# Kernel optimization log

Hardware: AMD Instinct MI355X
Metric: run time of the kernel (lower is better)

Reference implementation:

```python
import jax, jax.numpy as jnp
import numpy as np
from jax import lax

B, T = 32, 256
VOCAB, WDIM, MDIM = 50000, 300, 50
HID, NLAYERS, NCLASSES = 512, 2, 3


def _init(key, shape, scale):
    return (jax.random.normal(key, shape, dtype=jnp.float32) * scale)


def setup_inputs() -> dict:
    key = jax.random.key(0)
    ks = jax.random.split(key, 20)
    inputs_seq = jax.random.randint(ks[0], (B, T), 0, VOCAB, dtype=jnp.int32)
    masks = jax.random.randint(ks[1], (B, T), 0, 2, dtype=jnp.int32)
    length = jax.random.randint(ks[2], (B, 1), T // 2, T + 1, dtype=jnp.int32)
    embedding = _init(ks[3], (VOCAB, WDIM), 0.1)
    mask_embedding = _init(ks[4], (2, MDIM), 0.1)
    transition = _init(ks[5], (2, 2), 1.0)
    d_in0 = WDIM + MDIM          # 350
    d_in1 = 2 * HID              # 1024
    w_fw0 = _init(ks[6], (d_in0 + HID, 4 * HID), 0.02)
    b_fw0 = jnp.zeros((4 * HID,), jnp.float32)
    w_bw0 = _init(ks[7], (d_in0 + HID, 4 * HID), 0.02)
    b_bw0 = jnp.zeros((4 * HID,), jnp.float32)
    w_fw1 = _init(ks[8], (d_in1 + HID, 4 * HID), 0.02)
    b_fw1 = jnp.zeros((4 * HID,), jnp.float32)
    w_bw1 = _init(ks[9], (d_in1 + HID, 4 * HID), 0.02)
    b_bw1 = jnp.zeros((4 * HID,), jnp.float32)
    crf_w = _init(ks[10], (2 * HID, 2), 0.02)
    crf_b = jnp.zeros((2,), jnp.float32)
    logits_w = _init(ks[11], (2 * HID, NCLASSES), 0.02)
    logits_b = jnp.zeros((NCLASSES,), jnp.float32)
    return dict(inputs_seq=inputs_seq, masks=masks, length=length,
                embedding=embedding, mask_embedding=mask_embedding,
                transition=transition,
                w_fw0=w_fw0, b_fw0=b_fw0, w_bw0=w_bw0, b_bw0=b_bw0,
                w_fw1=w_fw1, b_fw1=b_fw1, w_bw1=w_bw1, b_bw1=b_bw1,
                crf_w=crf_w, crf_b=crf_b, logits_w=logits_w, logits_b=logits_b)


def _lstm_scan(x, length, W, b):
    """TF LSTMCell (gate order i, j, f, o; forget_bias=1.0) over time.
    Outputs are zeroed and state held past sequence_length (dynamic_rnn semantics)."""
    Bb, Tt, _ = x.shape
    H = W.shape[1] // 4
    zero = jnp.zeros((Bb, H), x.dtype)

    def step(carry, inp):
        h, c = carry
        xt, t = inp
        z = jnp.concatenate([xt, h], axis=-1) @ W + b
        i, j, f, o = jnp.split(z, 4, axis=-1)
        c_new = jax.nn.sigmoid(f + 1.0) * c + jax.nn.sigmoid(i) * jnp.tanh(j)
        h_new = jax.nn.sigmoid(o) * jnp.tanh(c_new)
        m = (t < length)[:, None]
        c = jnp.where(m, c_new, c)
        h = jnp.where(m, h_new, h)
        out = jnp.where(m, h_new, 0.0)
        return (h, c), out

    _, ys = lax.scan(step, (zero, zero), (x.transpose(1, 0, 2), jnp.arange(Tt)))
    return ys.transpose(1, 0, 2)  # [B,T,H]


def _reverse_seq(x, length):
    """tf.reverse_sequence along time: reverse first `length` steps, keep rest."""
    Tt = x.shape[1]
    t = jnp.arange(Tt)[None, :]
    L = length[:, None]
    idx = jnp.where(t < L, L - 1 - t, t)  # [B,T]
    return jnp.take_along_axis(x, idx[:, :, None], axis=1)


def _forward(inputs_seq, masks, length, embedding, mask_embedding, transition,
             lstm_params, crf_w, crf_b, logits_w, logits_b):
    length = length.reshape(-1)  # tf.squeeze
    emb = embedding[inputs_seq]          # [B,T,WDIM]
    memb = mask_embedding[masks]         # [B,T,MDIM]
    out = jnp.concatenate([emb, memb], axis=-1)
    for (wf, bf, wb, bb) in lstm_params:
        fw = _lstm_scan(out, length, wf, bf)
        bw = _reverse_seq(_lstm_scan(_reverse_seq(out, length), length, wb, bb), length)
        out = jnp.concatenate([fw, bw], axis=-1)  # [B,T,2H]

    # CRF forward probabilities over 2 tags
    e = out @ crf_w + crf_b              # [B,T,2] emission scores
    Tt = e.shape[1]
    alpha0 = e[:, 0]

    def crf_step(alpha, inp):
        et, t = inp
        new = jax.nn.logsumexp(alpha[:, :, None] + transition[None], axis=1) + et
        m = (t < length)[:, None]
        alpha = jnp.where(m, new, alpha)
        p = jnp.where(m, jax.nn.softmax(alpha, axis=-1), 0.0)
        return alpha, p

    _, probs_rest = lax.scan(crf_step, alpha0,
                             (e[:, 1:].transpose(1, 0, 2), jnp.arange(1, Tt)))
    p0 = jnp.where((length > 0)[:, None], jax.nn.softmax(alpha0, axis=-1), 0.0)
    probs = jnp.concatenate([p0[None], probs_rest], axis=0).transpose(1, 0, 2)  # [B,T,2]

    crf_out = probs[:, :, -1][:, None, :]            # [B,1,T]
    sentiment_vector = crf_out @ out                  # [B,1,2H]
    logits = jax.nn.softmax(sentiment_vector @ logits_w + logits_b, axis=-1)
    return logits  # [B,1,NCLASSES]


def reference(inputs_seq, masks, length, embedding, mask_embedding, transition,
              w_fw0, b_fw0, w_bw0, b_bw0, w_fw1, b_fw1, w_bw1, b_bw1,
              crf_w, crf_b, logits_w, logits_b):
    lstm_params = [(w_fw0, b_fw0, w_bw0, b_bw0), (w_fw1, b_fw1, w_bw1, b_bw1)]
    return _forward(inputs_seq, masks, length, embedding, mask_embedding,
                    transition, lstm_params, crf_w, crf_b, logits_w, logits_b)
```

## Files before the change

kernel.cpp:

```cpp
#include <hip/hip_runtime.h>
#include <hip/hip_bf16.h>
#include <cstdint>
#include <cstddef>

#define BB 32
#define TT 256
#define HID 512

typedef __attribute__((ext_vector_type(8))) short short8v;
typedef __attribute__((ext_vector_type(4))) float float4v;
typedef __attribute__((ext_vector_type(4))) unsigned int uint4v;

__device__ __forceinline__ float bf2f(unsigned short u) {
  return __uint_as_float(((unsigned int)u) << 16);
}
__device__ __forceinline__ unsigned short f2bf(float f) {
  unsigned int x = __float_as_uint(f);
  x += 0x7fffu + ((x >> 16) & 1u);
  return (unsigned short)(x >> 16);
}

__device__ __forceinline__ void stg4u_cohere(unsigned short* p, uint4v v) {
  asm volatile("global_store_dwordx4 %0, %1, off sc0 sc1"
               :: "v"(p), "v"(v) : "memory");
}
__device__ __forceinline__ void ldg4u_cohere_issue(uint4v& d, const unsigned short* p) {
  asm volatile("global_load_dwordx4 %0, %1, off sc0 sc1"
               : "=v"(d) : "v"(p) : "memory");
}
__device__ __forceinline__ void wait_vm0() {
  asm volatile("s_waitcnt vmcnt(0)" ::: "memory");
  __builtin_amdgcn_sched_barrier(0);
}

__global__ __launch_bounds__(256) void embed_kernel(
    const int* __restrict__ ids, const int* __restrict__ msk,
    const float* __restrict__ emb, const float* __restrict__ memb,
    unsigned short* __restrict__ x0b)
{
  int bt = blockIdx.x;
  int id = ids[bt];
  int m  = msk[bt];
  const float* er = emb  + (size_t)id * 300;
  const float* mr = memb + (size_t)m * 50;
  for (int d = threadIdx.x; d < 384; d += 256) {
    float v = (d < 300) ? er[d] : (d < 350 ? mr[d - 300] : 0.f);
    x0b[(size_t)bt * 384 + d] = f2bf(v);
  }
}

__global__ __launch_bounds__(256) void prep_w(
    const float* __restrict__ W, unsigned short* __restrict__ dst,
    int Kreal, int Kpad)
{
  __shared__ float tile[64][65];
  int tid = threadIdx.x;
  int n0 = blockIdx.x * 64;
  int k0 = blockIdx.y * 64;
#pragma unroll
  for (int i = 0; i < 4; ++i) {
    int e = tid + 256 * i;
    int r = e >> 4, c4 = (e & 15) * 4;
    float4 v = make_float4(0.f, 0.f, 0.f, 0.f);
    if (k0 + r < Kreal) v = *(const float4*)(W + (size_t)(k0 + r) * 2048 + n0 + c4);
    tile[r][c4 + 0] = v.x; tile[r][c4 + 1] = v.y;
    tile[r][c4 + 2] = v.z; tile[r][c4 + 3] = v.w;
  }
  __syncthreads();
  int nl = tid >> 2;
  int kg = (tid & 3) * 16;
  unsigned int pk[4], pk2[4];
#pragma unroll
  for (int jj = 0; jj < 4; ++jj) {
    unsigned short lo = f2bf(tile[kg + jj * 2 + 0][nl]);
    unsigned short hi = f2bf(tile[kg + jj * 2 + 1][nl]);
    pk[jj] = (unsigned int)lo | ((unsigned int)hi << 16);
  }
#pragma unroll
  for (int jj = 0; jj < 4; ++jj) {
    unsigned short lo = f2bf(tile[kg + 8 + jj * 2 + 0][nl]);
    unsigned short hi = f2bf(tile[kg + 8 + jj * 2 + 1][nl]);
    pk2[jj] = (unsigned int)lo | ((unsigned int)hi << 16);
  }
  size_t off = (size_t)(n0 + nl) * Kpad + k0 + kg;
  *(uint4*)(dst + off) = make_uint4(pk[0], pk[1], pk[2], pk[3]);
  *(uint4*)(dst + off + 8) = make_uint4(pk2[0], pk2[1], pk2[2], pk2[3]);
}

__global__ __launch_bounds__(256) void gemm_xproj(
    const unsigned short* __restrict__ A,
    const unsigned short* __restrict__ wxt,
    const float* __restrict__ bias,
    unsigned short* __restrict__ xq,
    int Kpad, int nkb)
{
  __shared__ unsigned short ws_s[128 * 64];
  __shared__ unsigned short xs_s[32 * 64];
  __shared__ float bias_s[128];
  int tid = threadIdx.x;
  int lane = tid & 63;
  int w = tid >> 6;
  int pos = blockIdx.x;
  int n0 = blockIdx.y * 128;
  if (tid < 128) bias_s[tid] = bias[n0 + tid];

  float4v acc[2][2];
#pragma unroll
  for (int i = 0; i < 2; ++i)
#pragma unroll
    for (int j = 0; j < 2; ++j) acc[i][j] = (float4v)0.f;

  int brow = tid >> 3;
  int seg = tid & 7;
  for (int kb = 0; kb < nkb; ++kb) {
    int k0 = kb * 64;
    __syncthreads();
    {
      const unsigned short* src = A + (size_t)(brow * 256 + pos) * Kpad + k0 + seg * 8;
      uint4 v = *(const uint4*)src;
      int o = (brow * 128 + seg * 16) ^ ((brow & 7) << 4);
      *(uint4*)((char*)xs_s + o) = v;
    }
#pragma unroll
    for (int i = 0; i < 4; ++i) {
      int n = i * 32 + brow;
      const unsigned short* src = wxt + (size_t)(n0 + n) * Kpad + k0 + seg * 8;
      uint4 v = *(const uint4*)src;
      int o = (n * 128 + seg * 16) ^ ((n & 7) << 4);
      *(uint4*)((char*)ws_s + o) = v;
    }
    __syncthreads();
#pragma unroll
    for (int kin = 0; kin < 64; kin += 32) {
      int kl = kin + ((lane >> 4) << 3);
      short8v afrag[2], bfrag[2];
#pragma unroll
      for (int nt = 0; nt < 2; ++nt) {
        int nl = w * 32 + nt * 16 + (lane & 15);
        int o = (nl * 128 + kl * 2) ^ ((nl & 7) << 4);
        afrag[nt] = *(const short8v*)((const char*)ws_s + o);
      }
#pragma unroll
      for (int bt = 0; bt < 2; ++bt) {
        int bl = bt * 16 + (lane & 15);
        int o = (bl * 128 + kl * 2) ^ ((bl & 7) << 4);
        bfrag[bt] = *(const short8v*)((const char*)xs_s + o);
      }
#pragma unroll
      for (int nt = 0; nt < 2; ++nt)
#pragma unroll
        for (int bt = 0; bt < 2; ++bt)
          acc[nt][bt] = __builtin_amdgcn_mfma_f32_16x16x32_bf16(
              afrag[nt], bfrag[bt], acc[nt][bt], 0, 0, 0);
    }
  }
  unsigned short* outp = xq + (size_t)pos * 65536;
#pragma unroll
  for (int nt = 0; nt < 2; ++nt) {
#pragma unroll
    for (int bt = 0; bt < 2; ++bt) {
#pragma unroll
      for (int reg = 0; reg < 4; ++reg) {
        int nl = w * 32 + nt * 16 + ((lane >> 4) << 2) + reg;
        int b = bt * 16 + (lane & 15);
        float v = acc[nt][bt][reg] + bias_s[nl];
        outp[(size_t)(n0 + nl) * 32 + b] = f2bf(v);
      }
    }
  }
}

__global__ __launch_bounds__(256) void lstm_mfma(
    const unsigned short* __restrict__ xq_fw, const unsigned short* __restrict__ xq_bw,
    const unsigned short* __restrict__ whT_fw, const unsigned short* __restrict__ whT_bw,
    const int* __restrict__ length,
    unsigned short* __restrict__ out,
    unsigned short* __restrict__ hT,
    float* __restrict__ cbuf,
    int* __restrict__ flags,
    int t0, int t1)
{
  extern __shared__ char smem[];
  float* zs = (float*)(smem + 65536);
  unsigned short* hb_st = (unsigned short*)(smem + 69632);
  unsigned short* ob_st = (unsigned short*)(smem + 70144);
  int tid = threadIdx.x;
  int wg = blockIdx.x;
  int dir = wg >> 6;
  int widx = wg & 63;
  int u0 = widx << 3;
  const unsigned short* xq = dir ? xq_bw : xq_fw;
  const unsigned short* whT = dir ? whT_bw : whT_fw;
  unsigned short* hbase = hT + (size_t)dir * 32768;
  int* dirflags = flags + dir * 2048;
  int* myflag = dirflags + widx * 32;

  {
    int r = tid >> 3;
    int q = r >> 3, d = r & 7;
    const unsigned short* src = whT + (size_t)(q * 512 + u0 + d) * 512 + (tid & 7) * 8;
    int ob = r * 1024 + (tid & 7) * 16;
    int sw = (r & 7) << 4;
#pragma unroll
    for (int i = 0; i < 8; ++i) {
      uint4 v = *(const uint4*)(src + i * 64);
      *(uint4*)(smem + ((ob + i * 128) ^ sw)) = v;
    }
  }

  int lane = tid & 63;
  int w = tid >> 6;
  int wr = w >> 1, wc = w & 1;
  int arow = wr * 16 + (lane & 15);
  int bcol = wc * 16 + (lane & 15);
  int chunk16 = (lane >> 4) << 4;
  int asw = (arow & 7) << 4;
  int bsw = (bcol & 7) << 4;
  int fu = tid >> 5;
  int fb = tid & 31;
  int ug = u0 + fu;
  int L = length[fb];
  float creg = 0.f;

  for (int t = t0; t < t1; ++t) {
    int sl = dir ? (TT - 1 - t) : t;
    const unsigned short* hTr_g = hbase + (size_t)(t & 1) * 16384;
    unsigned short* hTw_g = hbase + (size_t)((t & 1) ^ 1) * 16384;

    const unsigned short* xr = xq + (size_t)sl * 65536 + (size_t)ug * 32 + fb;
    float xv0 = bf2f(xr[0]);
    float xv1 = bf2f(xr[16384]);
    float xv2 = bf2f(xr[32768]);
    float xv3 = bf2f(xr[49152]);

    {
      int row = tid >> 3;
      const unsigned short* src = hTr_g + row * 512 + (tid & 7) * 8;
      uint4v r0, r1, r2, r3, r4, r5, r6, r7;
      ldg4u_cohere_issue(r0, src + 0 * 64);
      ldg4u_cohere_issue(r1, src + 1 * 64);
      ldg4u_cohere_issue(r2, src + 2 * 64);
      ldg4u_cohere_issue(r3, src + 3 * 64);
      ldg4u_cohere_issue(r4, src + 4 * 64);
      ldg4u_cohere_issue(r5, src + 5 * 64);
      ldg4u_cohere_issue(r6, src + 6 * 64);
      ldg4u_cohere_issue(r7, src + 7 * 64);
      wait_vm0();
      int ob = 32768 + row * 1024 + (tid & 7) * 16;
      int sw = (row & 7) << 4;
      *(uint4v*)(smem + ((ob + 0 * 128) ^ sw)) = r0;
      *(uint4v*)(smem + ((ob + 1 * 128) ^ sw)) = r1;
      *(uint4v*)(smem + ((ob + 2 * 128) ^ sw)) = r2;
      *(uint4v*)(smem + ((ob + 3 * 128) ^ sw)) = r3;
      *(uint4v*)(smem + ((ob + 4 * 128) ^ sw)) = r4;
      *(uint4v*)(smem + ((ob + 5 * 128) ^ sw)) = r5;
      *(uint4v*)(smem + ((ob + 6 * 128) ^ sw)) = r6;
      *(uint4v*)(smem + ((ob + 7 * 128) ^ sw)) = r7;
    }
    __syncthreads();

    float4v acc = (float4v)0.f;
#pragma unroll
    for (int ks = 0; ks < 16; ++ks) {
      int kb = ks * 64 + chunk16;
      short8v af = *(const short8v*)(smem + (size_t)arow * 1024 + (kb ^ asw));
      short8v bf = *(const short8v*)(smem + 32768 + (size_t)bcol * 1024 + (kb ^ bsw));
      acc = __builtin_amdgcn_mfma_f32_16x16x32_bf16(af, bf, acc, 0, 0, 0);
    }
#pragma unroll
    for (int r = 0; r < 4; ++r) {
      int row = wr * 16 + ((lane >> 4) << 2) + r;
      zs[row * 32 + bcol] = acc[r];
    }
    __syncthreads();

    {
      bool active = sl < L;
      float z0 = zs[(0 * 8 + fu) * 32 + fb] + xv0;
      float z1 = zs[(1 * 8 + fu) * 32 + fb] + xv1;
      float z2 = zs[(2 * 8 + fu) * 32 + fb] + xv2;
      float z3 = zs[(3 * 8 + fu) * 32 + fb] + xv3;
      int ho = 32768 + fb * 1024 + ((ug * 2) ^ ((fb & 7) << 4));
      float h_old = bf2f(*(const unsigned short*)(smem + ho));
      float c_old = cbuf ? cbuf[dir * 16384 + ug * 32 + fb] : creg;
      float si = 1.f / (1.f + expf(-z0));
      float sj = tanhf(z1);
      float sf = 1.f / (1.f + expf(-(z2 + 1.f)));
      float so = 1.f / (1.f + expf(-z3));
      float cn = sf * c_old + si * sj;
      float hn = so * tanhf(cn);
      if (active) {
        if (cbuf) cbuf[dir * 16384 + ug * 32 + fb] = cn; else creg = cn;
      }
      hb_st[fb * 8 + fu] = f2bf(active ? hn : h_old);
      ob_st[fb * 8 + fu] = f2bf(active ? hn : 0.f);
    }
    __syncthreads();

    if (tid < 32) {
      uint4v hv = *(const uint4v*)(hb_st + tid * 8);
      stg4u_cohere(hTw_g + tid * 512 + u0, hv);
      uint4v ov = *(const uint4v*)(ob_st + tid * 8);
      *(uint4v*)(out + (size_t)(tid * TT + sl) * 1024 + dir * 512 + u0) = ov;
    }

    if (t1 - t0 > 1) {
      wait_vm0();
      __syncthreads();
      if (tid == 0) {
        __hip_atomic_store(myflag, t + 1, __ATOMIC_RELAXED,
                           __HIP_MEMORY_SCOPE_AGENT);
      }
      if (tid < 64) {
        int* f = dirflags + tid * 32;
        while (__hip_atomic_load(f, __ATOMIC_RELAXED,
                                 __HIP_MEMORY_SCOPE_AGENT) < t + 1) {
          __builtin_amdgcn_s_sleep(1);
        }
      }
      __syncthreads();
    }
  }
}

__global__ __launch_bounds__(256) void crf_final(
    const unsigned short* __restrict__ out1,
    const float* __restrict__ crf_w, const float* __restrict__ crf_b,
    const float* __restrict__ trans,
    const int* __restrict__ length,
    const float* __restrict__ lw, const float* __restrict__ lb,
    float* __restrict__ dout)
{
  __shared__ float e[TT][2];
  __shared__ float pw[TT];
  __shared__ float sv[1024];
  __shared__ float red[256];
  int b = blockIdx.x, tid = threadIdx.x;
  int lane = tid & 63, w = tid >> 6;
  const unsigned short* ob = out1 + (size_t)b * TT * 1024;
  for (int t = w; t < TT; t += 4) {
    float a0 = 0.f, a1 = 0.f;
    for (int i = 0; i < 16; ++i) {
      int d = lane + i * 64;
      float v = bf2f(ob[(size_t)t * 1024 + d]);
      a0 += v * crf_w[d * 2];
      a1 += v * crf_w[d * 2 + 1];
    }
    for (int off = 32; off; off >>= 1) {
      a0 += __shfl_down(a0, off);
      a1 += __shfl_down(a1, off);
    }
    if (lane == 0) { e[t][0] = a0 + crf_b[0]; e[t][1] = a1 + crf_b[1]; }
  }
  __syncthreads();
  if (tid == 0) {
    int L = length[b];
    float t00 = trans[0], t01 = trans[1], t10 = trans[2], t11 = trans[3];
    float a0 = e[0][0], a1 = e[0][1];
    {
      float m = fmaxf(a0, a1);
      float e0 = expf(a0 - m), e1 = expf(a1 - m);
      pw[0] = (L > 0) ? (e1 / (e0 + e1)) : 0.f;
    }
    for (int t = 1; t < TT; ++t) {
      if (t < L) {
        float x0 = a0 + t00, y0 = a1 + t10;
        float m0 = fmaxf(x0, y0);
        float n0 = m0 + logf(expf(x0 - m0) + expf(y0 - m0)) + e[t][0];
        float x1 = a0 + t01, y1 = a1 + t11;
        float m1 = fmaxf(x1, y1);
        float n1 = m1 + logf(expf(x1 - m1) + expf(y1 - m1)) + e[t][1];
        a0 = n0; a1 = n1;
        float m = fmaxf(a0, a1);
        float e0 = expf(a0 - m), e1 = expf(a1 - m);
        pw[t] = e1 / (e0 + e1);
      } else {
        pw[t] = 0.f;
      }
    }
  }
  __syncthreads();
  for (int i = 0; i < 4; ++i) {
    int d = tid + i * 256;
    float s = 0.f;
    for (int t = 0; t < TT; ++t) s += pw[t] * bf2f(ob[(size_t)t * 1024 + d]);
    sv[d] = s;
  }
  __syncthreads();
  float v[3];
  for (int c = 0; c < 3; ++c) {
    float s = 0.f;
    for (int i = 0; i < 4; ++i) {
      int d = tid + i * 256;
      s += sv[d] * lw[d * 3 + c];
    }
    red[tid] = s;
    __syncthreads();
    for (int off = 128; off; off >>= 1) {
      if (tid < off) red[tid] += red[tid + off];
      __syncthreads();
    }
    if (tid == 0) v[c] = red[0] + lb[c];
    __syncthreads();
  }
  if (tid == 0) {
    float m = fmaxf(v[0], fmaxf(v[1], v[2]));
    float e0 = expf(v[0] - m), e1 = expf(v[1] - m), e2 = expf(v[2] - m);
    float s = e0 + e1 + e2;
    dout[b * 3 + 0] = e0 / s;
    dout[b * 3 + 1] = e1 / s;
    dout[b * 3 + 2] = e2 / s;
  }
}

#define LSTM_LDS 70656

static void run_layer(const unsigned short* xq_fw, const unsigned short* xq_bw,
                      const unsigned short* whT_fw, const unsigned short* whT_bw,
                      const int* len, unsigned short* out, unsigned short* hT,
                      float* cbuf_, int* flags, hipStream_t stream) {
  (void)hipMemsetAsync(hT, 0, 65536 * 2 + 32768 * 4 + 4096 * 4, stream);
  const unsigned short* a0 = xq_fw; const unsigned short* a1 = xq_bw;
  const unsigned short* a2 = whT_fw; const unsigned short* a3 = whT_bw;
  const int* a4 = len; unsigned short* a5 = out; unsigned short* a6 = hT;
  float* a7 = nullptr; int* a8 = flags; int a9 = 0, a10 = TT;
  void* args[11] = { &a0, &a1, &a2, &a3, &a4, &a5, &a6, &a7, &a8, &a9, &a10 };
  hipError_t err = hipLaunchCooperativeKernel(
      reinterpret_cast<const void*>(lstm_mfma), dim3(128), dim3(256),
      args, LSTM_LDS, stream);
  if (err != hipSuccess) {
    for (int t = 0; t < TT; ++t) {
      lstm_mfma<<<128, 256, LSTM_LDS, stream>>>(
          xq_fw, xq_bw, whT_fw, whT_bw, len, out, hT, cbuf_, flags, t, t + 1);
    }
  }
}

extern "C" void kernel_launch(void* const* d_in, const int* in_sizes, int n_in,
                              void* d_out, int out_size, void* d_ws, size_t ws_size,
                              hipStream_t stream) {
  (void)in_sizes; (void)n_in; (void)out_size; (void)ws_size;
  const int* ids    = (const int*)d_in[0];
  const int* msk    = (const int*)d_in[1];
  const int* len    = (const int*)d_in[2];
  const float* emb  = (const float*)d_in[3];
  const float* memb = (const float*)d_in[4];
  const float* trans= (const float*)d_in[5];
  const float* w_fw0= (const float*)d_in[6];
  const float* b_fw0= (const float*)d_in[7];
  const float* w_bw0= (const float*)d_in[8];
  const float* b_bw0= (const float*)d_in[9];
  const float* w_fw1= (const float*)d_in[10];
  const float* b_fw1= (const float*)d_in[11];
  const float* w_bw1= (const float*)d_in[12];
  const float* b_bw1= (const float*)d_in[13];
  const float* crf_w= (const float*)d_in[14];
  const float* crf_b= (const float*)d_in[15];
  const float* lw   = (const float*)d_in[16];
  const float* lb   = (const float*)d_in[17];
  float* outp = (float*)d_out;

  float* ws = (float*)d_ws;
  unsigned short* x0b   = (unsigned short*)(ws);
  unsigned short* wxt0f = (unsigned short*)(ws + 1572864);
  unsigned short* wxt0b = (unsigned short*)(ws + 1966080);
  unsigned short* wxt1f = (unsigned short*)(ws + 2359296);
  unsigned short* wxt1b = (unsigned short*)(ws + 3407872);
  unsigned short* whT0f = (unsigned short*)(ws + 4456448);
  unsigned short* whT0b = (unsigned short*)(ws + 4980736);
  unsigned short* whT1f = (unsigned short*)(ws + 5505024);
  unsigned short* whT1b = (unsigned short*)(ws + 6029312);
  unsigned short* xqf   = (unsigned short*)(ws + 6553600);
  unsigned short* xqb   = (unsigned short*)(ws + 14942208);
  unsigned short* out0b = (unsigned short*)(ws + 23330816);
  unsigned short* out1b = (unsigned short*)(ws + 27525120);
  unsigned short* hT    = (unsigned short*)(ws + 31719424);
  float* cbuf_ = ws + 31752192;
  int*   flags = (int*)(ws + 31784960);

  (void)hipFuncSetAttribute(reinterpret_cast<const void*>(lstm_mfma),
                            hipFuncAttributeMaxDynamicSharedMemorySize, LSTM_LDS);

  embed_kernel<<<8192, 256, 0, stream>>>(ids, msk, emb, memb, x0b);

  prep_w<<<dim3(32, 6), 256, 0, stream>>>(w_fw0, wxt0f, 350, 384);
  prep_w<<<dim3(32, 6), 256, 0, stream>>>(w_bw0, wxt0b, 350, 384);
  prep_w<<<dim3(32, 16), 256, 0, stream>>>(w_fw1, wxt1f, 1024, 1024);
  prep_w<<<dim3(32, 16), 256, 0, stream>>>(w_bw1, wxt1b, 1024, 1024);
  prep_w<<<dim3(32, 8), 256, 0, stream>>>(w_fw0 + (size_t)350 * 2048, whT0f, 512, 512);
  prep_w<<<dim3(32, 8), 256, 0, stream>>>(w_bw0 + (size_t)350 * 2048, whT0b, 512, 512);
  prep_w<<<dim3(32, 8), 256, 0, stream>>>(w_fw1 + (size_t)1024 * 2048, whT1f, 512, 512);
  prep_w<<<dim3(32, 8), 256, 0, stream>>>(w_bw1 + (size_t)1024 * 2048, whT1b, 512, 512);

  gemm_xproj<<<dim3(256, 16), 256, 0, stream>>>(x0b, wxt0f, b_fw0, xqf, 384, 6);
  gemm_xproj<<<dim3(256, 16), 256, 0, stream>>>(x0b, wxt0b, b_bw0, xqb, 384, 6);

  run_layer(xqf, xqb, whT0f, whT0b, len, out0b, hT, cbuf_, flags, stream);

  gemm_xproj<<<dim3(256, 16), 256, 0, stream>>>(out0b, wxt1f, b_fw1, xqf, 1024, 16);
  gemm_xproj<<<dim3(256, 16), 256, 0, stream>>>(out0b, wxt1b, b_bw1, xqb, 1024, 16);

  run_layer(xqf, xqb, whT1f, whT1b, len, out1b, hT, cbuf_, flags, stream);

  crf_final<<<32, 256, 0, stream>>>(out1b, crf_w, crf_b, trans, len, lw, lb, outp);
}
```

Before: 2.203 ms.

## Halve LSTM recurrent workgroups, each owning 16 hidden units, and trim the flag barrier

The persistent recurrent kernel now runs 64 workgroups instead of 128, each owning 16 hidden units (64 gate rows) instead of 8. Each wave issues two MFMAs per k-step and each thread computes two cells. This halves the number of workgroups that must spin on per-step flags and shortens the flag scan. The extra __syncthreads before signalling is dropped, and only the first wave waits for stores and polls flags. In exchange, each step does twice the MFMA and gate work per workgroup and needs more LDS, so per-step latency inside a workgroup may rise.

Result: slower. 2.518 ms (+14.3%).

```diff
diff --git a/kernel.cpp b/kernel.cpp
--- a/kernel.cpp
+++ b/kernel.cpp
@@ -181,57 +181,64 @@
     int t0, int t1)
 {
   extern __shared__ char smem[];
-  float* zs = (float*)(smem + 65536);
-  unsigned short* hb_st = (unsigned short*)(smem + 69632);
-  unsigned short* ob_st = (unsigned short*)(smem + 70144);
+  float* zs = (float*)(smem + 98304);
+  unsigned short* hb_st = (unsigned short*)(smem + 106496);
+  unsigned short* ob_st = (unsigned short*)(smem + 107520);
   int tid = threadIdx.x;
   int wg = blockIdx.x;
-  int dir = wg >> 6;
-  int widx = wg & 63;
-  int u0 = widx << 3;
+  int dir = wg >> 5;
+  int widx = wg & 31;
+  int u0 = widx << 4;
   const unsigned short* xq = dir ? xq_bw : xq_fw;
   const unsigned short* whT = dir ? whT_bw : whT_fw;
   unsigned short* hbase = hT + (size_t)dir * 32768;
-  int* dirflags = flags + dir * 2048;
+  int* dirflags = flags + dir * 1024;
   int* myflag = dirflags + widx * 32;
 
   {
-    int r = tid >> 3;
-    int q = r >> 3, d = r & 7;
-    const unsigned short* src = whT + (size_t)(q * 512 + u0 + d) * 512 + (tid & 7) * 8;
-    int ob = r * 1024 + (tid & 7) * 16;
-    int sw = (r & 7) << 4;
-#pragma unroll
-    for (int i = 0; i < 8; ++i) {
-      uint4 v = *(const uint4*)(src + i * 64);
-      *(uint4*)(smem + ((ob + i * 128) ^ sw)) = v;
+    int seg = tid & 7;
+    int rbase = tid >> 3;
+#pragma unroll
+    for (int rr = 0; rr < 2; ++rr) {
+      int r = rr * 32 + rbase;
+      int q = r >> 4, d = r & 15;
+      const unsigned short* src = whT + (size_t)(q * 512 + u0 + d) * 512 + seg * 8;
+      int ob = r * 1024 + seg * 16;
+      int sw = (r & 7) << 4;
+#pragma unroll
+      for (int i = 0; i < 8; ++i) {
+        uint4 v = *(const uint4*)(src + i * 64);
+        *(uint4*)(smem + ((ob + i * 128) ^ sw)) = v;
+      }
     }
   }
 
   int lane = tid & 63;
   int w = tid >> 6;
-  int wr = w >> 1, wc = w & 1;
-  int arow = wr * 16 + (lane & 15);
-  int bcol = wc * 16 + (lane & 15);
+  int arow = w * 16 + (lane & 15);
   int chunk16 = (lane >> 4) << 4;
   int asw = (arow & 7) << 4;
+  int bcol = lane & 15;
   int bsw = (bcol & 7) << 4;
   int fu = tid >> 5;
   int fb = tid & 31;
-  int ug = u0 + fu;
   int L = length[fb];
-  float creg = 0.f;
+  float creg[2] = {0.f, 0.f};
 
   for (int t = t0; t < t1; ++t) {
     int sl = dir ? (TT - 1 - t) : t;
     const unsigned short* hTr_g = hbase + (size_t)(t & 1) * 16384;
     unsigned short* hTw_g = hbase + (size_t)((t & 1) ^ 1) * 16384;
 
-    const unsigned short* xr = xq + (size_t)sl * 65536 + (size_t)ug * 32 + fb;
-    float xv0 = bf2f(xr[0]);
-    float xv1 = bf2f(xr[16384]);
-    float xv2 = bf2f(xr[32768]);
-    float xv3 = bf2f(xr[49152]);
+    float xv[2][4];
+    {
+      const unsigned short* xr = xq + (size_t)sl * 65536 + (size_t)(u0 + fu) * 32 + fb;
+#pragma unroll
+      for (int uu = 0; uu < 2; ++uu)
+#pragma unroll
+        for (int q = 0; q < 4; ++q)
+          xv[uu][q] = bf2f(xr[uu * 256 + q * 16384]);
+    }
 
     {
       int row = tid >> 3;
@@ -246,7 +253,7 @@
       ldg4u_cohere_issue(r6, src + 6 * 64);
       ldg4u_cohere_issue(r7, src + 7 * 64);
       wait_vm0();
-      int ob = 32768 + row * 1024 + (tid & 7) * 16;
+      int ob = 65536 + row * 1024 + (tid & 7) * 16;
       int sw = (row & 7) << 4;
       *(uint4v*)(smem + ((ob + 0 * 128) ^ sw)) = r0;
       *(uint4v*)(smem + ((ob + 1 * 128) ^ sw)) = r1;
@@ -259,30 +266,36 @@
     }
     __syncthreads();
 
-    float4v acc = (float4v)0.f;
+    float4v acc0 = (float4v)0.f, acc1 = (float4v)0.f;
 #pragma unroll
     for (int ks = 0; ks < 16; ++ks) {
       int kb = ks * 64 + chunk16;
       short8v af = *(const short8v*)(smem + (size_t)arow * 1024 + (kb ^ asw));
-      short8v bf = *(const short8v*)(smem + 32768 + (size_t)bcol * 1024 + (kb ^ bsw));
-      acc = __builtin_amdgcn_mfma_f32_16x16x32_bf16(af, bf, acc, 0, 0, 0);
+      short8v bf0 = *(const short8v*)(smem + 65536 + (size_t)bcol * 1024 + (kb ^ bsw));
+      short8v bf1 = *(const short8v*)(smem + 65536 + (size_t)(bcol + 16) * 1024 + (kb ^ bsw));
+      acc0 = __builtin_amdgcn_mfma_f32_16x16x32_bf16(af, bf0, acc0, 0, 0, 0);
+      acc1 = __builtin_amdgcn_mfma_f32_16x16x32_bf16(af, bf1, acc1, 0, 0, 0);
     }
 #pragma unroll
     for (int r = 0; r < 4; ++r) {
-      int row = wr * 16 + ((lane >> 4) << 2) + r;
-      zs[row * 32 + bcol] = acc[r];
-    }
-    __syncthreads();
-
-    {
-      bool active = sl < L;
-      float z0 = zs[(0 * 8 + fu) * 32 + fb] + xv0;
-      float z1 = zs[(1 * 8 + fu) * 32 + fb] + xv1;
-      float z2 = zs[(2 * 8 + fu) * 32 + fb] + xv2;
-      float z3 = zs[(3 * 8 + fu) * 32 + fb] + xv3;
-      int ho = 32768 + fb * 1024 + ((ug * 2) ^ ((fb & 7) << 4));
+      int row = w * 16 + ((lane >> 4) << 2) + r;
+      zs[row * 32 + bcol] = acc0[r];
+      zs[row * 32 + bcol + 16] = acc1[r];
+    }
+    __syncthreads();
+
+    bool active = sl < L;
+#pragma unroll
+    for (int uu = 0; uu < 2; ++uu) {
+      int du = fu + uu * 8;
+      int ug = u0 + du;
+      float z0 = zs[(0 * 16 + du) * 32 + fb] + xv[uu][0];
+      float z1 = zs[(1 * 16 + du) * 32 + fb] + xv[uu][1];
+      float z2 = zs[(2 * 16 + du) * 32 + fb] + xv[uu][2];
+      float z3 = zs[(3 * 16 + du) * 32 + fb] + xv[uu][3];
+      int ho = 65536 + fb * 1024 + ((ug * 2) ^ ((fb & 7) << 4));
       float h_old = bf2f(*(const unsigned short*)(smem + ho));
-      float c_old = cbuf ? cbuf[dir * 16384 + ug * 32 + fb] : creg;
+      float c_old = cbuf ? cbuf[dir * 16384 + ug * 32 + fb] : creg[uu];
       float si = 1.f / (1.f + expf(-z0));
       float sj = tanhf(z1);
       float sf = 1.f / (1.f + expf(-(z2 + 1.f)));
@@ -290,32 +303,40 @@
       float cn = sf * c_old + si * sj;
       float hn = so * tanhf(cn);
       if (active) {
-        if (cbuf) cbuf[dir * 16384 + ug * 32 + fb] = cn; else creg = cn;
-      }
-      hb_st[fb * 8 + fu] = f2bf(active ? hn : h_old);
-      ob_st[fb * 8 + fu] = f2bf(active ? hn : 0.f);
+        if (cbuf) cbuf[dir * 16384 + ug * 32 + fb] = cn; else creg[uu] = cn;
+      }
+      hb_st[fb * 16 + du] = f2bf(active ? hn : h_old);
+      ob_st[fb * 16 + du] = f2bf(active ? hn : 0.f);
     }
     __syncthreads();
 
     if (tid < 32) {
-      uint4v hv = *(const uint4v*)(hb_st + tid * 8);
-      stg4u_cohere(hTw_g + tid * 512 + u0, hv);
-      uint4v ov = *(const uint4v*)(ob_st + tid * 8);
-      *(uint4v*)(out + (size_t)(tid * TT + sl) * 1024 + dir * 512 + u0) = ov;
+      uint4v h0 = *(const uint4v*)(hb_st + tid * 16);
+      uint4v h1 = *(const uint4v*)(hb_st + tid * 16 + 8);
+      stg4u_cohere(hTw_g + tid * 512 + u0, h0);
+      stg4u_cohere(hTw_g + tid * 512 + u0 + 8, h1);
+    } else if (tid >= 64 && tid < 96) {
+      int b = tid - 64;
+      uint4v o0 = *(const uint4v*)(ob_st + b * 16);
+      uint4v o1 = *(const uint4v*)(ob_st + b * 16 + 8);
+      unsigned short* op = out + (size_t)(b * TT + sl) * 1024 + dir * 512 + u0;
+      *(uint4v*)op = o0;
+      *(uint4v*)(op + 8) = o1;
     }
 
     if (t1 - t0 > 1) {
-      wait_vm0();
-      __syncthreads();
-      if (tid == 0) {
-        __hip_atomic_store(myflag, t + 1, __ATOMIC_RELAXED,
-                           __HIP_MEMORY_SCOPE_AGENT);
-      }
       if (tid < 64) {
-        int* f = dirflags + tid * 32;
-        while (__hip_atomic_load(f, __ATOMIC_RELAXED,
-                                 __HIP_MEMORY_SCOPE_AGENT) < t + 1) {
-          __builtin_amdgcn_s_sleep(1);
+        wait_vm0();
+        if (tid == 0) {
+          __hip_atomic_store(myflag, t + 1, __ATOMIC_RELAXED,
+                             __HIP_MEMORY_SCOPE_AGENT);
+        }
+        if (tid < 32) {
+          int* f = dirflags + tid * 32;
+          while (__hip_atomic_load(f, __ATOMIC_RELAXED,
+                                   __HIP_MEMORY_SCOPE_AGENT) < t + 1) {
+            __builtin_amdgcn_s_sleep(1);
+          }
         }
       }
       __syncthreads();
@@ -413,24 +434,24 @@
   }
 }
 
-#define LSTM_LDS 70656
+#define LSTM_LDS 108544
 
 static void run_layer(const unsigned short* xq_fw, const unsigned short* xq_bw,
                       const unsigned short* whT_fw, const unsigned short* whT_bw,
                       const int* len, unsigned short* out, unsigned short* hT,
                       float* cbuf_, int* flags, hipStream_t stream) {
-  (void)hipMemsetAsync(hT, 0, 65536 * 2 + 32768 * 4 + 4096 * 4, stream);
+  (void)hipMemsetAsync(hT, 0, 131072 + 131072 + 8192, stream);
   const unsigned short* a0 = xq_fw; const unsigned short* a1 = xq_bw;
   const unsigned short* a2 = whT_fw; const unsigned short* a3 = whT_bw;
   const int* a4 = len; unsigned short* a5 = out; unsigned short* a6 = hT;
   float* a7 = nullptr; int* a8 = flags; int a9 = 0, a10 = TT;
   void* args[11] = { &a0, &a1, &a2, &a3, &a4, &a5, &a6, &a7, &a8, &a9, &a10 };
   hipError_t err = hipLaunchCooperativeKernel(
-      reinterpret_cast<const void*>(lstm_mfma), dim3(128), dim3(256),
+      reinterpret_cast<const void*>(lstm_mfma), dim3(64), dim3(256),
       args, LSTM_LDS, stream);
   if (err != hipSuccess) {
     for (int t = 0; t < TT; ++t) {
-      lstm_mfma<<<128, 256, LSTM_LDS, stream>>>(
+      lstm_mfma<<<64, 256, LSTM_LDS, stream>>>(
           xq_fw, xq_bw, whT_fw, whT_bw, len, out, hT, cbuf_, flags, t, t + 1);
     }
   }
```
